# Kernel optimization log

Measured on AMD Instinct MI355X. Metric: run time of the kernel, lower is better.

## Reference

```python
import jax, jax.numpy as jnp
import numpy as np


def positional_encoding(n_tokens, d_model, dtype=jnp.float32):
    # standard sinusoidal PE: pe[pos, 2i] = sin(pos / 10000^(2i/d)), pe[pos, 2i+1] = cos(...)
    pos = jnp.arange(n_tokens, dtype=dtype)[:, None]            # [n, 1]
    i = jnp.arange(0, d_model, 2, dtype=dtype)[None, :]         # [1, d/2]
    angle = pos / jnp.power(jnp.asarray(10000.0, dtype), i / d_model)
    pe = jnp.zeros((n_tokens, d_model), dtype)
    pe = pe.at[:, 0::2].set(jnp.sin(angle))
    pe = pe.at[:, 1::2].set(jnp.cos(angle))
    return pe


def layer_norm(x, gamma, beta, eps=1e-5):
    mu = jnp.mean(x, axis=-1, keepdims=True)
    var = jnp.var(x, axis=-1, keepdims=True)
    return (x - mu) * jax.lax.rsqrt(var + eps) * gamma + beta


def setup_inputs() -> dict:
    key = jax.random.key(0)
    ks = jax.random.split(key, 4)
    b, n, d = 4, 1024, 1024
    dh = 1024  # dim_hidden_linear
    s = 1.0 / np.sqrt(d)
    return {
        "token_embedding": jax.random.normal(ks[0], (b, n, d), jnp.float32),
        "ln_gamma": jnp.ones((d,), jnp.float32),
        "ln_beta": jnp.zeros((d,), jnp.float32),
        "Wq": jax.random.normal(ks[1], (d, dh), jnp.float32) * s,
        "bq": jnp.zeros((dh,), jnp.float32),
        "Wk": jax.random.normal(ks[2], (d, dh), jnp.float32) * s,
        "bk": jnp.zeros((dh,), jnp.float32),
        "Wv": jax.random.normal(ks[3], (d, dh), jnp.float32) * s,
        "bv": jnp.zeros((dh,), jnp.float32),
        "num_heads": 16,
    }


def reference(token_embedding, ln_gamma, ln_beta, Wq, bq, Wk, bk, Wv, bv, num_heads):
    b, n, d = token_embedding.shape
    pe = positional_encoding(n, d)                      # [n, d]
    x = token_embedding + pe[None, :, :]                # broadcast over batch
    x = layer_norm(x, ln_gamma, ln_beta)
    q = x @ Wq + bq                                     # [b, n, dh]
    k = x @ Wk + bk
    v = x @ Wv + bv
    dh = q.shape[-1]
    hd = dh // num_heads                                # per-head dim
    q = q.reshape(b, n, num_heads, hd)
    k = k.reshape(b, n, num_heads, hd)
    v = v.reshape(b, n, num_heads, hd)
    scale = 1.0 / jnp.sqrt(jnp.asarray(hd, q.dtype))
    scores = jnp.einsum("bqhd,bkhd->bhqk", q, k) * scale  # [b, h, n, n]
    attn = jax.nn.softmax(scores, axis=-1)
    out = jnp.einsum("bhqk,bkhd->bqhd", attn, v)          # [b, n, h, hd]
    return out.reshape(b, n, dh)
```

## Files before the change

### kernel.cpp

```cpp
#include <hip/hip_runtime.h>
#include <hip/hip_bf16.h>
#include <math.h>

typedef __attribute__((ext_vector_type(8))) short bf16x8;
typedef __attribute__((ext_vector_type(4))) float f32x4;
typedef __attribute__((ext_vector_type(16))) float f32x16;

static __device__ __forceinline__ void gld16(const void* g, void* l) {
    __builtin_amdgcn_global_load_lds(
        (const __attribute__((address_space(1))) unsigned int*)g,
        (__attribute__((address_space(3))) unsigned int*)l, 16, 0, 0);
}

static __device__ __forceinline__ unsigned cvtpk(float lo, float hi) {
    unsigned r;
    asm("v_cvt_pk_bf16_f32 %0, %1, %2" : "=v"(r) : "v"(lo), "v"(hi));
    return r;
}

__global__ __launch_bounds__(256) void peln_wt_kernel(
    const float* __restrict__ emb,
    const float* __restrict__ gamma,
    const float* __restrict__ beta,
    const float* __restrict__ Wq,
    const float* __restrict__ Wk,
    const float* __restrict__ Wv,
    __hip_bfloat16* __restrict__ x,
    __hip_bfloat16* __restrict__ Wt)
{
    const int tid = threadIdx.x;
    if (blockIdx.x < 4096) {
        const int row = blockIdx.x;
        const int t   = row & 1023;
        float4 e = ((const float4*)(emb + (size_t)row * 1024))[tid];
        float v[4] = {e.x, e.y, e.z, e.w};
        float s = 0.f, ss = 0.f;
        #pragma unroll
        for (int kk = 0; kk < 4; ++kk) {
            int c = tid * 4 + kk;
            float ang = (float)t * exp2f(-13.287712379549449f * (float)(c >> 1) * (1.0f / 512.0f));
            float pe  = (c & 1) ? __cosf(ang) : __sinf(ang);
            v[kk] += pe;
            s  += v[kk];
            ss += v[kk] * v[kk];
        }
        #pragma unroll
        for (int off = 1; off < 64; off <<= 1) {
            s  += __shfl_xor(s, off);
            ss += __shfl_xor(ss, off);
        }
        __shared__ float red_s[4], red_ss[4];
        int wave = tid >> 6, lane = tid & 63;
        if (lane == 0) { red_s[wave] = s; red_ss[wave] = ss; }
        __syncthreads();
        float S  = red_s[0] + red_s[1] + red_s[2] + red_s[3];
        float SS = red_ss[0] + red_ss[1] + red_ss[2] + red_ss[3];
        float mu   = S * (1.0f / 1024.0f);
        float var  = SS * (1.0f / 1024.0f) - mu * mu;
        float rstd = rsqrtf(var + 1e-5f);
        #pragma unroll
        for (int kk = 0; kk < 4; ++kk) {
            int c = tid * 4 + kk;
            float y = (v[kk] - mu) * rstd * gamma[c] + beta[c];
            x[(size_t)row * 1024 + c] = __float2bfloat16(y);
        }
    } else {
        __shared__ __hip_bfloat16 tile[32][33];
        int wid = blockIdx.x - 4096;
        int zz  = wid >> 10;
        int rem = wid & 1023;
        int bx = rem & 31, by = rem >> 5;
        int tx = tid & 31, ty = tid >> 5;
        const float* src = (zz == 0) ? Wq : (zz == 1) ? Wk : Wv;
        __hip_bfloat16* dst = Wt + (size_t)zz * 1024 * 1024;
        int x0 = bx * 32, y0 = by * 32;
        #pragma unroll
        for (int kk = 0; kk < 4; ++kk)
            tile[ty + 8 * kk][tx] =
                __float2bfloat16(src[(size_t)(y0 + ty + 8 * kk) * 1024 + x0 + tx]);
        __syncthreads();
        #pragma unroll
        for (int kk = 0; kk < 4; ++kk)
            dst[(size_t)(x0 + ty + 8 * kk) * 1024 + y0 + tx] = tile[tx][ty + 8 * kk];
    }
}

__global__ __launch_bounds__(256) void qkv_gemm(
    const __hip_bfloat16* __restrict__ X,
    const __hip_bfloat16* __restrict__ Wt,
    const float* __restrict__ bq,
    const float* __restrict__ bk,
    const float* __restrict__ bv,
    __hip_bfloat16* __restrict__ qkv,
    __hip_bfloat16* __restrict__ vt)
{
    union SMem {
        struct { __hip_bfloat16 A[128 * 64]; __hip_bfloat16 B[128 * 64]; } s;
        __hip_bfloat16 C[128 * 132];
    };
    __shared__ __align__(16) SMem sm;

    const int id   = blockIdx.x;
    const int xcd  = id & 7;
    const int rest = id >> 3;
    const int j    = rest % 3;
    const int mblk = rest / 3;
    const int m0   = mblk * 128;
    const int n0   = (xcd * 3 + j) * 128;
    const int t    = n0 >> 10;
    const int nn0  = n0 & 1023;
    const __hip_bfloat16* W = Wt + (size_t)t * 1024 * 1024;

    const int tid  = threadIdx.x;
    const int wave = tid >> 6, lane = tid & 63;
    const int wm = wave & 1, wn = wave >> 1;
    const int lm = lane & 15, quad = lane >> 4;

    const int srow = lane >> 3;
    const int skc  = ((lane & 7) ^ srow) * 8;
    const int rbase = wave * 32;
    const __hip_bfloat16* gA = X + (size_t)(m0 + rbase + srow) * 1024 + skc;
    const __hip_bfloat16* gB = W + (size_t)(nn0 + rbase + srow) * 1024 + skc;
    __hip_bfloat16* lA = sm.s.A + rbase * 64;
    __hip_bfloat16* lB = sm.s.B + rbase * 64;

    f32x4 acc[4][4];
    #pragma unroll
    for (int i = 0; i < 4; ++i)
        #pragma unroll
        for (int jj = 0; jj < 4; ++jj)
            acc[i][jj] = (f32x4){0.f, 0.f, 0.f, 0.f};

    #pragma unroll
    for (int n = 0; n < 4; ++n) {
        gld16(gA + (size_t)n * 8 * 1024, lA + n * 8 * 64);
        gld16(gB + (size_t)n * 8 * 1024, lB + n * 8 * 64);
    }

    for (int k0 = 0; k0 < 1024; k0 += 64) {
        __syncthreads();

        bf16x8 a[2][4], b[2][4];
        #pragma unroll
        for (int ks = 0; ks < 2; ++ks) {
            #pragma unroll
            for (int i = 0; i < 4; ++i) {
                int row = wm * 64 + i * 16 + lm;
                a[ks][i] = *(const bf16x8*)(sm.s.A + (size_t)row * 64
                                            + (((ks * 4 + quad) ^ (lm & 7)) * 8));
            }
            #pragma unroll
            for (int jj = 0; jj < 4; ++jj) {
                int row = wn * 64 + jj * 16 + lm;
                b[ks][jj] = *(const bf16x8*)(sm.s.B + (size_t)row * 64
                                             + (((ks * 4 + quad) ^ (lm & 7)) * 8));
            }
        }
        __syncthreads();

        if (k0 + 64 < 1024) {
            #pragma unroll
            for (int n = 0; n < 4; ++n) {
                gld16(gA + (size_t)n * 8 * 1024 + k0 + 64, lA + n * 8 * 64);
                gld16(gB + (size_t)n * 8 * 1024 + k0 + 64, lB + n * 8 * 64);
            }
        }

        #pragma unroll
        for (int ks = 0; ks < 2; ++ks)
            #pragma unroll
            for (int i = 0; i < 4; ++i)
                #pragma unroll
                for (int jj = 0; jj < 4; ++jj)
                    acc[i][jj] = __builtin_amdgcn_mfma_f32_16x16x32_bf16(a[ks][i], b[ks][jj], acc[i][jj], 0, 0, 0);
    }

    const float* bias = (t == 0) ? bq : (t == 1) ? bk : bv;
    if (t < 2) {
        #pragma unroll
        for (int jj = 0; jj < 4; ++jj) {
            int col = wn * 64 + jj * 16 + lm;
            float bb = bias[nn0 + col];
            #pragma unroll
            for (int i = 0; i < 4; ++i)
                #pragma unroll
                for (int r = 0; r < 4; ++r) {
                    int row = wm * 64 + i * 16 + quad * 4 + r;
                    sm.C[(size_t)row * 132 + col] = __float2bfloat16(acc[i][jj][r] + bb);
                }
        }
        __syncthreads();
        __hip_bfloat16* out = qkv + (size_t)t * 4096 * 1024;
        #pragma unroll
        for (int c = 0; c < 8; ++c) {
            int g = tid + 256 * c;
            int row = g >> 4;
            int colc = (g & 15) * 8;
            bf16x8 vch = *(const bf16x8*)&sm.C[(size_t)row * 132 + colc];
            *(bf16x8*)(out + (size_t)(m0 + row) * 1024 + nn0 + colc) = vch;
        }
    } else {
        #pragma unroll
        for (int jj = 0; jj < 4; ++jj) {
            int col = wn * 64 + jj * 16 + lm;
            float bb = bias[nn0 + col];
            #pragma unroll
            for (int i = 0; i < 4; ++i)
                #pragma unroll
                for (int r = 0; r < 4; ++r) {
                    int row = wm * 64 + i * 16 + quad * 4 + r;
                    sm.C[(size_t)col * 132 + row] = __float2bfloat16(acc[i][jj][r] + bb);
                }
        }
        __syncthreads();
        const int bbase = (m0 >> 10) * 16 + (nn0 >> 6);
        const int mloc  = m0 & 1023;
        #pragma unroll
        for (int c = 0; c < 8; ++c) {
            int g = tid + 256 * c;
            int col = g >> 4;
            int rch = (g & 15) * 8;
            bf16x8 vch = *(const bf16x8*)&sm.C[(size_t)col * 132 + rch];
            int bh = bbase + (col >> 6);
            int d  = col & 63;
            *(bf16x8*)(vt + ((size_t)bh * 64 + d) * 1024 + mloc + rch) = vch;
        }
    }
}

__global__ __launch_bounds__(256, 2) void attn_kernel(
    const __hip_bfloat16* __restrict__ q,
    const __hip_bfloat16* __restrict__ k,
    const __hip_bfloat16* __restrict__ vt,
    float* __restrict__ out)
{
    const int id   = blockIdx.x;
    const int bh   = (id & 7) * 8 + ((id >> 3) & 7);
    const int qblk = id >> 6;
    const int b = bh >> 4, h = bh & 15;
    const int wave = threadIdx.x >> 6, lane = threadIdx.x & 63;
    const int l31 = lane & 31, hi5 = lane >> 5;
    const int qbase = qblk * 128 + wave * 32;
    const float CEXP = 0.18033688011112042f;

    bf16x8 bq32[4];
    #pragma unroll
    for (int slab = 0; slab < 4; ++slab)
        bq32[slab] = *(const bf16x8*)(q + (size_t)(b * 1024 + qbase + l31) * 1024
                                        + h * 64 + (slab * 2 + hi5) * 8);

    const __hip_bfloat16* kg = k + (size_t)(b * 1024) * 1024 + h * 64;
    const __hip_bfloat16* vg = vt + (size_t)bh * 64 * 1024;

    f32x16 OT[2];
    #pragma unroll
    for (int dt = 0; dt < 2; ++dt)
        #pragma unroll
        for (int r = 0; r < 16; ++r)
            OT[dt][r] = 0.f;
    float li = 0.f;

    for (int kc = 0; kc < 1024; kc += 64) {
        f32x16 ST[2];
        #pragma unroll
        for (int kt = 0; kt < 2; ++kt) {
            #pragma unroll
            for (int r = 0; r < 16; ++r) ST[kt][r] = 0.f;
            #pragma unroll
            for (int slab = 0; slab < 4; ++slab) {
                bf16x8 ak = *(const bf16x8*)(kg
                    + (size_t)(kc + kt * 32 + l31) * 1024
                    + (slab * 2 + hi5) * 8);
                ST[kt] = __builtin_amdgcn_mfma_f32_32x32x16_bf16(ak, bq32[slab], ST[kt], 0, 0, 0);
            }
        }

        unsigned pw[4][4];
        #pragma unroll
        for (int kt = 0; kt < 2; ++kt) {
            float pv[16];
            #pragma unroll
            for (int r = 0; r < 16; ++r) {
                pv[r] = __builtin_amdgcn_exp2f(ST[kt][r] * CEXP);
                li += pv[r];
            }
            #pragma unroll
            for (int s = 0; s < 2; ++s) {
                unsigned P0 = cvtpk(pv[8 * s + 0], pv[8 * s + 1]);
                unsigned P1 = cvtpk(pv[8 * s + 2], pv[8 * s + 3]);
                unsigned P2 = cvtpk(pv[8 * s + 4], pv[8 * s + 5]);
                unsigned P3 = cvtpk(pv[8 * s + 6], pv[8 * s + 7]);
                asm("v_permlane32_swap_b32 %0, %1" : "+v"(P0), "+v"(P2));
                asm("v_permlane32_swap_b32 %0, %1" : "+v"(P1), "+v"(P3));
                int ks = kt * 2 + s;
                pw[ks][0] = P0; pw[ks][1] = P1; pw[ks][2] = P2; pw[ks][3] = P3;
            }
        }

        #pragma unroll
        for (int dt = 0; dt < 2; ++dt)
            #pragma unroll
            for (int ks = 0; ks < 4; ++ks) {
                bf16x8 av = *(const bf16x8*)(vg
                    + (size_t)(dt * 32 + l31) * 1024
                    + kc + (ks * 2 + hi5) * 8);
                bf16x8 pf;
                __builtin_memcpy(&pf, pw[ks], 16);
                OT[dt] = __builtin_amdgcn_mfma_f32_32x32x16_bf16(av, pf, OT[dt], 0, 0, 0);
            }
    }

    li += __shfl_xor(li, 32);
    float inv = 1.0f / li;
    const int qrow = qbase + l31;

    #pragma unroll
    for (int dt = 0; dt < 2; ++dt)
        #pragma unroll
        for (int g = 0; g < 4; ++g) {
            float4 o4 = {OT[dt][4 * g + 0] * inv, OT[dt][4 * g + 1] * inv,
                         OT[dt][4 * g + 2] * inv, OT[dt][4 * g + 3] * inv};
            *(float4*)(out + (size_t)(b * 1024 + qrow) * 1024
                       + h * 64 + dt * 32 + 8 * g + 4 * hi5) = o4;
        }
}

extern "C" void kernel_launch(void* const* d_in, const int* in_sizes, int n_in,
                              void* d_out, int out_size, void* d_ws, size_t ws_size,
                              hipStream_t stream)
{
    const float* emb   = (const float*)d_in[0];
    const float* gamma = (const float*)d_in[1];
    const float* beta  = (const float*)d_in[2];
    const float* Wq    = (const float*)d_in[3];
    const float* bq    = (const float*)d_in[4];
    const float* Wk    = (const float*)d_in[5];
    const float* bk    = (const float*)d_in[6];
    const float* Wv    = (const float*)d_in[7];
    const float* bv    = (const float*)d_in[8];
    float* out = (float*)d_out;

    __hip_bfloat16* ws  = (__hip_bfloat16*)d_ws;
    __hip_bfloat16* x   = ws;
    __hip_bfloat16* Wt  = x   + (size_t)4096 * 1024;
    __hip_bfloat16* qkv = Wt  + (size_t)3 * 1024 * 1024;
    __hip_bfloat16* vt  = qkv + (size_t)2 * 4096 * 1024;

    peln_wt_kernel<<<4096 + 3072, 256, 0, stream>>>(emb, gamma, beta, Wq, Wk, Wv, x, Wt);
    qkv_gemm<<<768, 256, 0, stream>>>(x, Wt, bq, bk, bv, qkv, vt);
    attn_kernel<<<512, 256, 0, stream>>>(qkv, qkv + (size_t)4096 * 1024, vt, out);
}
```

Measured before the change: 184.1 us.

## Stage K/V tiles in LDS with double buffering and switch attention to 16x16 MFMA

```diff
diff --git a/kernel.cpp b/kernel.cpp
--- a/kernel.cpp
+++ b/kernel.cpp
@@ -3,8 +3,8 @@
 #include <math.h>
 
 typedef __attribute__((ext_vector_type(8))) short bf16x8;
+typedef __attribute__((ext_vector_type(4))) short bf16x4;
 typedef __attribute__((ext_vector_type(4))) float f32x4;
-typedef __attribute__((ext_vector_type(16))) float f32x16;
 
 static __device__ __forceinline__ void gld16(const void* g, void* l) {
     __builtin_amdgcn_global_load_lds(
@@ -12,10 +12,11 @@
         (__attribute__((address_space(3))) unsigned int*)l, 16, 0, 0);
 }
 
-static __device__ __forceinline__ unsigned cvtpk(float lo, float hi) {
-    unsigned r;
-    asm("v_cvt_pk_bf16_f32 %0, %1, %2" : "=v"(r) : "v"(lo), "v"(hi));
-    return r;
+static __device__ __forceinline__ short f2bf_s(float f) {
+    __hip_bfloat16 h = __float2bfloat16(f);
+    short s;
+    __builtin_memcpy(&s, &h, 2);
+    return s;
 }
 
 __global__ __launch_bounds__(256) void peln_wt_kernel(
@@ -228,101 +229,116 @@
     }
 }
 
-__global__ __launch_bounds__(256, 2) void attn_kernel(
+__global__ __launch_bounds__(256, 4) void attn_kernel(
     const __hip_bfloat16* __restrict__ q,
     const __hip_bfloat16* __restrict__ k,
     const __hip_bfloat16* __restrict__ vt,
     float* __restrict__ out)
 {
+    __shared__ __align__(16) __hip_bfloat16 Kbuf[2][64 * 64];
+    __shared__ __align__(16) __hip_bfloat16 Vbuf[2][64 * 64];
+    __shared__ short ldsPT[4][16 * 64];
     const int id   = blockIdx.x;
     const int bh   = (id & 7) * 8 + ((id >> 3) & 7);
     const int qblk = id >> 6;
     const int b = bh >> 4, h = bh & 15;
     const int wave = threadIdx.x >> 6, lane = threadIdx.x & 63;
-    const int l31 = lane & 31, hi5 = lane >> 5;
-    const int qbase = qblk * 128 + wave * 32;
+    const int lm = lane & 15, quad = lane >> 4;
+    const int qbase = qblk * 64 + wave * 16;
     const float CEXP = 0.18033688011112042f;
 
-    bf16x8 bq32[4];
-    #pragma unroll
-    for (int slab = 0; slab < 4; ++slab)
-        bq32[slab] = *(const bf16x8*)(q + (size_t)(b * 1024 + qbase + l31) * 1024
-                                        + h * 64 + (slab * 2 + hi5) * 8);
+    bf16x8 bqf[2];
+    #pragma unroll
+    for (int ks = 0; ks < 2; ++ks)
+        bqf[ks] = *(const bf16x8*)(q + (size_t)(b * 1024 + qbase + lm) * 1024
+                                     + h * 64 + ks * 32 + quad * 8);
 
     const __hip_bfloat16* kg = k + (size_t)(b * 1024) * 1024 + h * 64;
     const __hip_bfloat16* vg = vt + (size_t)bh * 64 * 1024;
-
-    f32x16 OT[2];
-    #pragma unroll
-    for (int dt = 0; dt < 2; ++dt)
-        #pragma unroll
-        for (int r = 0; r < 16; ++r)
-            OT[dt][r] = 0.f;
+    const int srow = lane >> 3;
+    const int skc  = ((lane & 7) ^ srow) * 8;
+
+    f32x4 OT[4];
+    #pragma unroll
+    for (int dt = 0; dt < 4; ++dt)
+        OT[dt] = (f32x4){0.f, 0.f, 0.f, 0.f};
     float li = 0.f;
 
-    for (int kc = 0; kc < 1024; kc += 64) {
-        f32x16 ST[2];
-        #pragma unroll
-        for (int kt = 0; kt < 2; ++kt) {
-            #pragma unroll
-            for (int r = 0; r < 16; ++r) ST[kt][r] = 0.f;
-            #pragma unroll
-            for (int slab = 0; slab < 4; ++slab) {
-                bf16x8 ak = *(const bf16x8*)(kg
-                    + (size_t)(kc + kt * 32 + l31) * 1024
-                    + (slab * 2 + hi5) * 8);
-                ST[kt] = __builtin_amdgcn_mfma_f32_32x32x16_bf16(ak, bq32[slab], ST[kt], 0, 0, 0);
-            }
-        }
-
-        unsigned pw[4][4];
-        #pragma unroll
-        for (int kt = 0; kt < 2; ++kt) {
-            float pv[16];
-            #pragma unroll
-            for (int r = 0; r < 16; ++r) {
-                pv[r] = __builtin_amdgcn_exp2f(ST[kt][r] * CEXP);
-                li += pv[r];
-            }
-            #pragma unroll
-            for (int s = 0; s < 2; ++s) {
-                unsigned P0 = cvtpk(pv[8 * s + 0], pv[8 * s + 1]);
-                unsigned P1 = cvtpk(pv[8 * s + 2], pv[8 * s + 3]);
-                unsigned P2 = cvtpk(pv[8 * s + 4], pv[8 * s + 5]);
-                unsigned P3 = cvtpk(pv[8 * s + 6], pv[8 * s + 7]);
-                asm("v_permlane32_swap_b32 %0, %1" : "+v"(P0), "+v"(P2));
-                asm("v_permlane32_swap_b32 %0, %1" : "+v"(P1), "+v"(P3));
-                int ks = kt * 2 + s;
-                pw[ks][0] = P0; pw[ks][1] = P1; pw[ks][2] = P2; pw[ks][3] = P3;
-            }
-        }
-
-        #pragma unroll
-        for (int dt = 0; dt < 2; ++dt)
-            #pragma unroll
-            for (int ks = 0; ks < 4; ++ks) {
-                bf16x8 av = *(const bf16x8*)(vg
-                    + (size_t)(dt * 32 + l31) * 1024
-                    + kc + (ks * 2 + hi5) * 8);
-                bf16x8 pf;
-                __builtin_memcpy(&pf, pw[ks], 16);
-                OT[dt] = __builtin_amdgcn_mfma_f32_32x32x16_bf16(av, pf, OT[dt], 0, 0, 0);
-            }
-    }
-
+    auto stageKV = [&](int buf, int kt0) {
+        #pragma unroll
+        for (int n = 0; n < 2; ++n) {
+            int r0 = wave * 16 + n * 8;
+            gld16(kg + (size_t)(kt0 + r0 + srow) * 1024 + skc, Kbuf[buf] + r0 * 64);
+        }
+        #pragma unroll
+        for (int n = 0; n < 2; ++n) {
+            int d0 = wave * 16 + n * 8;
+            gld16(vg + (size_t)(d0 + srow) * 1024 + kt0 + skc, Vbuf[buf] + d0 * 64);
+        }
+    };
+
+    stageKV(0, 0);
+
+    for (int tt = 0; tt < 16; ++tt) {
+        __syncthreads();
+        if (tt + 1 < 16) stageKV((tt + 1) & 1, (tt + 1) * 64);
+
+        const __hip_bfloat16* Kb = Kbuf[tt & 1];
+        const __hip_bfloat16* Vb = Vbuf[tt & 1];
+
+        f32x4 ST[4];
+        #pragma unroll
+        for (int kt = 0; kt < 4; ++kt) {
+            ST[kt] = (f32x4){0.f, 0.f, 0.f, 0.f};
+            #pragma unroll
+            for (int ks = 0; ks < 2; ++ks) {
+                bf16x8 ak = *(const bf16x8*)(Kb + (size_t)(kt * 16 + lm) * 64
+                                             + (((ks * 4 + quad) ^ (lm & 7)) * 8));
+                ST[kt] = __builtin_amdgcn_mfma_f32_16x16x32_bf16(ak, bqf[ks], ST[kt], 0, 0, 0);
+            }
+        }
+
+        #pragma unroll
+        for (int kt = 0; kt < 4; ++kt) {
+            bf16x4 pk;
+            #pragma unroll
+            for (int r = 0; r < 4; ++r) {
+                float p = __builtin_amdgcn_exp2f(ST[kt][r] * CEXP);
+                li += p;
+                pk[r] = f2bf_s(p);
+            }
+            int u = kt * 2 + (quad >> 1);
+            *(bf16x4*)&ldsPT[wave][lm * 64 + ((u ^ (lm & 7)) << 3) + (quad & 1) * 4] = pk;
+        }
+
+        bf16x8 bp[2];
+        #pragma unroll
+        for (int ks = 0; ks < 2; ++ks)
+            bp[ks] = *(const bf16x8*)&ldsPT[wave][lm * 64
+                      + (((ks * 4 + quad) ^ (lm & 7)) << 3)];
+
+        #pragma unroll
+        for (int dt = 0; dt < 4; ++dt)
+            #pragma unroll
+            for (int ks = 0; ks < 2; ++ks) {
+                bf16x8 av = *(const bf16x8*)(Vb + (size_t)(dt * 16 + lm) * 64
+                                             + (((ks * 4 + quad) ^ (lm & 7)) * 8));
+                OT[dt] = __builtin_amdgcn_mfma_f32_16x16x32_bf16(av, bp[ks], OT[dt], 0, 0, 0);
+            }
+    }
+
+    li += __shfl_xor(li, 16);
     li += __shfl_xor(li, 32);
     float inv = 1.0f / li;
-    const int qrow = qbase + l31;
-
-    #pragma unroll
-    for (int dt = 0; dt < 2; ++dt)
-        #pragma unroll
-        for (int g = 0; g < 4; ++g) {
-            float4 o4 = {OT[dt][4 * g + 0] * inv, OT[dt][4 * g + 1] * inv,
-                         OT[dt][4 * g + 2] * inv, OT[dt][4 * g + 3] * inv};
-            *(float4*)(out + (size_t)(b * 1024 + qrow) * 1024
-                       + h * 64 + dt * 32 + 8 * g + 4 * hi5) = o4;
-        }
+    const int qrow = qbase + lm;
+
+    #pragma unroll
+    for (int dt = 0; dt < 4; ++dt) {
+        float4 o4 = {OT[dt][0] * inv, OT[dt][1] * inv,
+                     OT[dt][2] * inv, OT[dt][3] * inv};
+        *(float4*)(out + (size_t)(b * 1024 + qrow) * 1024
+                   + h * 64 + dt * 16 + quad * 4) = o4;
+    }
 }
 
 extern "C" void kernel_launch(void* const* d_in, const int* in_sizes, int n_in,
@@ -348,5 +364,5 @@
 
     peln_wt_kernel<<<4096 + 3072, 256, 0, stream>>>(emb, gamma, beta, Wq, Wk, Wv, x, Wt);
     qkv_gemm<<<768, 256, 0, stream>>>(x, Wt, bq, bk, bv, qkv, vt);
-    attn_kernel<<<512, 256, 0, stream>>>(qkv, qkv + (size_t)4096 * 1024, vt, out);
-}
+    attn_kernel<<<1024, 256, 0, stream>>>(qkv, qkv + (size_t)4096 * 1024, vt, out);
+}
```

Measured after the change: 151.7 us. -17.6%, faster.

## Store K and V in MFMA-fragment tiled layout for contiguous attention loads

Applied to the files above, without the earlier changes.

```diff
diff --git a/kernel.cpp b/kernel.cpp
--- a/kernel.cpp
+++ b/kernel.cpp
@@ -190,14 +190,33 @@
                 }
         }
         __syncthreads();
-        __hip_bfloat16* out = qkv + (size_t)t * 4096 * 1024;
-        #pragma unroll
-        for (int c = 0; c < 8; ++c) {
-            int g = tid + 256 * c;
-            int row = g >> 4;
-            int colc = (g & 15) * 8;
-            bf16x8 vch = *(const bf16x8*)&sm.C[(size_t)row * 132 + colc];
-            *(bf16x8*)(out + (size_t)(m0 + row) * 1024 + nn0 + colc) = vch;
+        if (t == 0) {
+            __hip_bfloat16* outq = qkv;
+            #pragma unroll
+            for (int c = 0; c < 8; ++c) {
+                int g = tid + 256 * c;
+                int row = g >> 4;
+                int colc = (g & 15) * 8;
+                bf16x8 vch = *(const bf16x8*)&sm.C[(size_t)row * 132 + colc];
+                *(bf16x8*)(outq + (size_t)(m0 + row) * 1024 + nn0 + colc) = vch;
+            }
+        } else {
+            __hip_bfloat16* kk = qkv + (size_t)4096 * 1024;
+            const int b_ = m0 >> 10;
+            #pragma unroll
+            for (int c = 0; c < 8; ++c) {
+                int g = tid + 256 * c;
+                int row = g >> 4;
+                int colc = (g & 15) * 8;
+                bf16x8 vch = *(const bf16x8*)&sm.C[(size_t)row * 132 + colc];
+                int key = (m0 & 1023) + row;
+                int gcol = nn0 + colc;
+                int bh = b_ * 16 + (gcol >> 6);
+                int d = gcol & 63;
+                size_t off = ((((size_t)bh * 32 + (key >> 5)) * 4 + (d >> 4)) * 32
+                              + (key & 31)) * 16 + (d & 15);
+                *(bf16x8*)(kk + off) = vch;
+            }
         }
     } else {
         #pragma unroll
@@ -213,24 +232,27 @@
                 }
         }
         __syncthreads();
-        const int bbase = (m0 >> 10) * 16 + (nn0 >> 6);
-        const int mloc  = m0 & 1023;
+        const int b_ = m0 >> 10;
         #pragma unroll
         for (int c = 0; c < 8; ++c) {
             int g = tid + 256 * c;
             int col = g >> 4;
             int rch = (g & 15) * 8;
             bf16x8 vch = *(const bf16x8*)&sm.C[(size_t)col * 132 + rch];
-            int bh = bbase + (col >> 6);
-            int d  = col & 63;
-            *(bf16x8*)(vt + ((size_t)bh * 64 + d) * 1024 + mloc + rch) = vch;
+            int dg = nn0 + col;
+            int bh = b_ * 16 + (dg >> 6);
+            int d = dg & 63;
+            int key = (m0 & 1023) + rch;
+            size_t off = ((((size_t)bh * 2 + (d >> 5)) * 64 + (key >> 4)) * 32
+                          + (d & 31)) * 16 + (key & 15);
+            *(bf16x8*)(vt + off) = vch;
         }
     }
 }
 
 __global__ __launch_bounds__(256, 2) void attn_kernel(
     const __hip_bfloat16* __restrict__ q,
-    const __hip_bfloat16* __restrict__ k,
+    const __hip_bfloat16* __restrict__ kk,
     const __hip_bfloat16* __restrict__ vt,
     float* __restrict__ out)
 {
@@ -249,8 +271,8 @@
         bq32[slab] = *(const bf16x8*)(q + (size_t)(b * 1024 + qbase + l31) * 1024
                                         + h * 64 + (slab * 2 + hi5) * 8);
 
-    const __hip_bfloat16* kg = k + (size_t)(b * 1024) * 1024 + h * 64;
-    const __hip_bfloat16* vg = vt + (size_t)bh * 64 * 1024;
+    const __hip_bfloat16* Kt = kk + (size_t)bh * 65536;
+    const __hip_bfloat16* Vt = vt + (size_t)bh * 65536;
 
     f32x16 OT[2];
     #pragma unroll
@@ -268,9 +290,9 @@
             for (int r = 0; r < 16; ++r) ST[kt][r] = 0.f;
             #pragma unroll
             for (int slab = 0; slab < 4; ++slab) {
-                bf16x8 ak = *(const bf16x8*)(kg
-                    + (size_t)(kc + kt * 32 + l31) * 1024
-                    + (slab * 2 + hi5) * 8);
+                bf16x8 ak = *(const bf16x8*)(Kt
+                    + ((((size_t)(kc >> 5) + kt) * 4 + slab) * 32 + l31) * 16
+                    + hi5 * 8);
                 ST[kt] = __builtin_amdgcn_mfma_f32_32x32x16_bf16(ak, bq32[slab], ST[kt], 0, 0, 0);
             }
         }
@@ -301,9 +323,9 @@
         for (int dt = 0; dt < 2; ++dt)
             #pragma unroll
             for (int ks = 0; ks < 4; ++ks) {
-                bf16x8 av = *(const bf16x8*)(vg
-                    + (size_t)(dt * 32 + l31) * 1024
-                    + kc + (ks * 2 + hi5) * 8);
+                bf16x8 av = *(const bf16x8*)(Vt
+                    + (((size_t)dt * 64 + (kc >> 4) + ks) * 32 + l31) * 16
+                    + hi5 * 8);
                 bf16x8 pf;
                 __builtin_memcpy(&pf, pw[ks], 16);
                 OT[dt] = __builtin_amdgcn_mfma_f32_32x32x16_bf16(av, pf, OT[dt], 0, 0, 0);
```

Result: faster. 148.5 us (-19.3%).
